# Kernel optimization log

Measured on AMD Instinct MI355X. Metric: run time of the kernel, lower is better.

## Reference

```python
import jax, jax.numpy as jnp
import numpy as np

N_ITER, K, DIM = 2, 16, 64


def setup_inputs() -> dict:
    key = jax.random.key(0)
    ks = jax.random.split(key, 9)
    B, NE, NU, NR = 8192, 200000, 100000, 32
    return {
        "u": jax.random.randint(ks[0], (B,), 0, NU),
        "v": jax.random.randint(ks[1], (B,), 0, NE),
        "adj_ent": jax.random.randint(ks[2], (NE, K), 0, NE),
        "adj_rel": jax.random.randint(ks[3], (NE, K), 0, NR),
        "usr_emb": jax.random.normal(ks[4], (NU, DIM), jnp.float32) * 0.1,
        "rel_emb": jax.random.normal(ks[5], (NR, DIM), jnp.float32) * 0.1,
        "ent_emb": jax.random.normal(ks[6], (NE, DIM), jnp.float32) * 0.1,
        "W": jax.random.normal(ks[7], (DIM, DIM), jnp.float32) / np.float32(np.sqrt(DIM)),
        "b": jnp.zeros((DIM,), jnp.float32),
    }


def reference(u, v, adj_ent, adj_rel, usr_emb, rel_emb, ent_emb, W, b):
    B = u.shape[0]
    user = usr_emb[u]                                  # [B, D]

    # _get_neighbors: multi-hop fixed-fanout expansion
    entities = [v[:, None]]                            # hop 0: [B, 1]
    relations = []
    for h in range(N_ITER):
        entities.append(adj_ent[entities[h]].reshape(B, -1))   # [B, K^(h+1)]
        relations.append(adj_rel[entities[h]].reshape(B, -1))

    ent_vecs = [ent_emb[e] for e in entities]          # [B, K^h, D] gathers
    rel_vecs = [rel_emb[r] for r in relations]

    # _aggregate: attention-weighted neighbor mix + sum-combine linear
    for i in range(N_ITER):
        act = jnp.tanh if i == N_ITER - 1 else jax.nn.sigmoid
        nxt = []
        for hop in range(N_ITER - i):
            self_v = ent_vecs[hop]                              # [B, m, D]
            neigh = ent_vecs[hop + 1].reshape(B, -1, K, DIM)    # [B, m, K, D]
            rel = rel_vecs[hop].reshape(B, -1, K, DIM)          # [B, m, K, D]
            scores = jnp.einsum('bd,bmkd->bmk', user, rel)      # user-relation
            attn = jax.nn.softmax(scores, axis=-1)              # [B, m, K]
            agg = jnp.einsum('bmk,bmkd->bmd', attn, neigh)      # weighted sum
            nxt.append(act((self_v + agg) @ W + b))             # sum aggregator
        ent_vecs = nxt

    item = ent_vecs[0].reshape(B, DIM)
    return jax.nn.sigmoid(jnp.sum(user * item, axis=1))        # [B]
```

## Files before the change

### kernel.cpp

```cpp
#include <hip/hip_runtime.h>

#define KF    16
#define DIM   64
#define BLOCK 256

typedef __attribute__((ext_vector_type(8))) short bs8;
typedef __attribute__((ext_vector_type(4))) float f32x4;

__device__ __forceinline__ float fsig(float x) {
    return __builtin_amdgcn_rcpf(1.0f + __expf(-x));
}
__device__ __forceinline__ float ftanh(float x) {
    float e = __expf(2.0f * x);
    return 1.0f - 2.0f * __builtin_amdgcn_rcpf(e + 1.0f);
}
__device__ __forceinline__ ushort f2bf(float x) {
    uint u = __builtin_bit_cast(uint, x);
    u += 0x7fffu + ((u >> 16) & 1u);
    return (ushort)(u >> 16);
}

__global__ __launch_bounds__(BLOCK) void kgcn_kernel(
    const int* __restrict__ u, const int* __restrict__ v,
    const int* __restrict__ adj_ent, const int* __restrict__ adj_rel,
    const float* __restrict__ usr_emb, const float* __restrict__ rel_emb,
    const float* __restrict__ ent_emb, const float* __restrict__ W,
    const float* __restrict__ bias, float* __restrict__ out, int B)
{
    __shared__ float b_l[DIM];
    __shared__ float urs_l[32];
    __shared__ int   e1l[KF];
    __shared__ float at1l[KF];
    __shared__ int   e2l[4][64];
    __shared__ float at2l[4][64];
    __shared__ __align__(16) ushort Xl[16][72];
    __shared__ float part0[4][DIM];
    __shared__ float xbuf[DIM];
    __shared__ float agg2s[DIM];
    __shared__ float psum[4];

    const int tid  = threadIdx.x;
    const int lane = tid & 63;
    const int wv   = tid >> 6;
    const int b    = blockIdx.x;
    const int lr   = lane & 15;
    const int lg   = lane >> 4;
    const int col  = wv * 16 + lr;

    bs8 wf0, wf1;
    #pragma unroll
    for (int i = 0; i < 8; ++i) {
        const int k = lg * 8 + i;
        wf0[i] = (short)f2bf(W[k * DIM + col]);
        wf1[i] = (short)f2bf(W[(k + 32) * DIM + col]);
    }
    if (tid < DIM) b_l[tid] = bias[tid];

    const int e0 = v[b];
    float user = 0.0f, ent0v = 0.0f;

    if (wv == 0) {
        user  = usr_emb[(size_t)u[b] * DIM + lane];
        ent0v = ent_emb[(size_t)e0 * DIM + lane];
        xbuf[lane] = user;
        const int r = lane & 31, h = lane >> 5;
        float s = 0.0f;
        #pragma unroll
        for (int dd = 0; dd < 32; ++dd) {
            const int d = h * 32 + dd;
            s += xbuf[d] * rel_emb[r * DIM + d];
        }
        s += __shfl_xor(s, 32);
        if (lane < 32) urs_l[lane] = s;
        const int k  = lane & 15;
        const int e1 = adj_ent[e0 * KF + k];
        const int r1 = adj_rel[e0 * KF + k];
        float sc = urs_l[r1];
        float mx = sc;
        mx = fmaxf(mx, __shfl_xor(mx, 1));
        mx = fmaxf(mx, __shfl_xor(mx, 2));
        mx = fmaxf(mx, __shfl_xor(mx, 4));
        mx = fmaxf(mx, __shfl_xor(mx, 8));
        float e  = __expf(sc - mx);
        float sm = e;
        sm += __shfl_xor(sm, 1);
        sm += __shfl_xor(sm, 2);
        sm += __shfl_xor(sm, 4);
        sm += __shfl_xor(sm, 8);
        if (lane < KF) { e1l[lane] = e1; at1l[lane] = e * __builtin_amdgcn_rcpf(sm); }
    }
    __syncthreads();

    {
        const int mm = wv * 4 + lg;
        const int em = e1l[mm];
        const int e2 = adj_ent[em * KF + lr];
        float sc = urs_l[adj_rel[em * KF + lr]];
        float mx = sc;
        mx = fmaxf(mx, __shfl_xor(mx, 1));
        mx = fmaxf(mx, __shfl_xor(mx, 2));
        mx = fmaxf(mx, __shfl_xor(mx, 4));
        mx = fmaxf(mx, __shfl_xor(mx, 8));
        float e  = __expf(sc - mx);
        float sm = e;
        sm += __shfl_xor(sm, 1);
        sm += __shfl_xor(sm, 2);
        sm += __shfl_xor(sm, 4);
        sm += __shfl_xor(sm, 8);
        e2l[wv][lane]  = e2;
        at2l[wv][lane] = e * __builtin_amdgcn_rcpf(sm);
    }

    float agg0p = 0.0f;
    #pragma unroll 1
    for (int q = 0; q < 4; ++q) {
        const int m = wv * 4 + q;
        float rows[KF + 1];
        #pragma unroll
        for (int k = 0; k < KF; ++k) {
            const int e = __builtin_amdgcn_readfirstlane(e2l[wv][q * 16 + k]);
            rows[k] = ent_emb[(size_t)e * DIM + lane];
        }
        const int es = __builtin_amdgcn_readfirstlane(e1l[m]);
        rows[KF] = ent_emb[(size_t)es * DIM + lane];

        float g0 = 0.0f, g1 = 0.0f, g2 = 0.0f, g3 = 0.0f;
        #pragma unroll
        for (int k = 0; k < KF; k += 4) {
            g0 = fmaf(at2l[wv][q * 16 + k + 0], rows[k + 0], g0);
            g1 = fmaf(at2l[wv][q * 16 + k + 1], rows[k + 1], g1);
            g2 = fmaf(at2l[wv][q * 16 + k + 2], rows[k + 2], g2);
            g3 = fmaf(at2l[wv][q * 16 + k + 3], rows[k + 3], g3);
        }
        const float selfv = rows[KF];
        const float x     = selfv + ((g0 + g1) + (g2 + g3));
        agg0p = fmaf(at1l[m], selfv, agg0p);
        Xl[m][lane] = f2bf(x);
    }
    part0[wv][lane] = agg0p;
    __syncthreads();

    const float bj = b_l[col];
    f32x4 c; c[0] = bj; c[1] = bj; c[2] = bj; c[3] = bj;
    {
        const ushort* arow = &Xl[lr][lg * 8];
        bs8 a0 = *(const bs8*)arow;
        bs8 a1 = *(const bs8*)(arow + 32);
        c = __builtin_amdgcn_mfma_f32_16x16x32_bf16(a0, wf0, c, 0, 0, 0);
        c = __builtin_amdgcn_mfma_f32_16x16x32_bf16(a1, wf1, c, 0, 0, 0);
    }
    {
        float p = 0.0f;
        #pragma unroll
        for (int r = 0; r < 4; ++r) p = fmaf(at1l[lg * 4 + r], fsig(c[r]), p);
        p += __shfl_xor(p, 16);
        p += __shfl_xor(p, 32);
        if (lane < 16) agg2s[col] = p;
    }
    __syncthreads();

    if (wv == 0) {
        const float agg0 = (part0[0][lane] + part0[1][lane]) + (part0[2][lane] + part0[3][lane]);
        Xl[0][lane] = f2bf(ent0v + agg0);
    }
    __syncthreads();

    c[0] = bj; c[1] = bj; c[2] = bj; c[3] = bj;
    {
        const ushort* arow = &Xl[lr][lg * 8];
        bs8 a0 = *(const bs8*)arow;
        bs8 a1 = *(const bs8*)(arow + 32);
        c = __builtin_amdgcn_mfma_f32_16x16x32_bf16(a0, wf0, c, 0, 0, 0);
        c = __builtin_amdgcn_mfma_f32_16x16x32_bf16(a1, wf1, c, 0, 0, 0);
    }
    __syncthreads();
    if (lane < 16) {
        const float h0 = fsig(c[0]);
        Xl[0][col] = f2bf(h0 + agg2s[col]);
    }
    __syncthreads();

    c[0] = bj; c[1] = bj; c[2] = bj; c[3] = bj;
    {
        const ushort* arow = &Xl[lr][lg * 8];
        bs8 a0 = *(const bs8*)arow;
        bs8 a1 = *(const bs8*)(arow + 32);
        c = __builtin_amdgcn_mfma_f32_16x16x32_bf16(a0, wf0, c, 0, 0, 0);
        c = __builtin_amdgcn_mfma_f32_16x16x32_bf16(a1, wf1, c, 0, 0, 0);
    }
    float pv = 0.0f;
    if (lane < 16) pv = xbuf[col] * ftanh(c[0]);
    pv += __shfl_xor(pv, 1);
    pv += __shfl_xor(pv, 2);
    pv += __shfl_xor(pv, 4);
    pv += __shfl_xor(pv, 8);
    pv += __shfl_xor(pv, 16);
    pv += __shfl_xor(pv, 32);
    if (lane == 0) psum[wv] = pv;
    __syncthreads();
    if (tid == 0) out[b] = fsig((psum[0] + psum[1]) + (psum[2] + psum[3]));
}

extern "C" void kernel_launch(void* const* d_in, const int* in_sizes, int n_in,
                              void* d_out, int out_size, void* d_ws, size_t ws_size,
                              hipStream_t stream) {
    const int*   u       = (const int*)d_in[0];
    const int*   v       = (const int*)d_in[1];
    const int*   adj_ent = (const int*)d_in[2];
    const int*   adj_rel = (const int*)d_in[3];
    const float* usr_emb = (const float*)d_in[4];
    const float* rel_emb = (const float*)d_in[5];
    const float* ent_emb = (const float*)d_in[6];
    const float* W       = (const float*)d_in[7];
    const float* bias    = (const float*)d_in[8];
    float* out = (float*)d_out;

    const int B = in_sizes[0];
    kgcn_kernel<<<B, BLOCK, 0, stream>>>(u, v, adj_ent, adj_rel,
                                         usr_emb, rel_emb, ent_emb,
                                         W, bias, out, B);
}
```

Measured before the change: 203.0 us.

## Process one batch element per wavefront with register-resident softmax and shared W fragments

Remaps the kernel so each 256-thread block handles four batch elements, one per wavefront, and launches B/4 blocks. Each wave keeps its own neighbor ids and attention weights in registers, reading them with readlane and shuffles instead of LDS, and runs all four output-column MFMA tiles itself. W is converted to bf16 fragments once per block into shared memory and reused by all four waves. This removes most block-wide barriers and the per-element W conversion and LDS traffic. In exchange each wave does more serial gather and MFMA work, and the grid has a quarter as many blocks. The launch assumes B is divisible by 4.

```diff
diff --git a/kernel.cpp b/kernel.cpp
--- a/kernel.cpp
+++ b/kernel.cpp
@@ -6,6 +6,8 @@
 
 typedef __attribute__((ext_vector_type(8))) short bs8;
 typedef __attribute__((ext_vector_type(4))) float f32x4;
+
+#define C_FENCE() asm volatile("" ::: "memory")
 
 __device__ __forceinline__ float fsig(float x) {
     return __builtin_amdgcn_rcpf(1.0f + __expf(-x));
@@ -18,6 +20,9 @@
     uint u = __builtin_bit_cast(uint, x);
     u += 0x7fffu + ((u >> 16) & 1u);
     return (ushort)(u >> 16);
+}
+__device__ __forceinline__ float rdlane_f(float v, int l) {
+    return __builtin_bit_cast(float, __builtin_amdgcn_readlane(__builtin_bit_cast(int, v), l));
 }
 
 __global__ __launch_bounds__(BLOCK) void kgcn_kernel(
@@ -27,55 +32,51 @@
     const float* __restrict__ ent_emb, const float* __restrict__ W,
     const float* __restrict__ bias, float* __restrict__ out, int B)
 {
-    __shared__ float b_l[DIM];
-    __shared__ float urs_l[32];
-    __shared__ int   e1l[KF];
-    __shared__ float at1l[KF];
-    __shared__ int   e2l[4][64];
-    __shared__ float at2l[4][64];
-    __shared__ __align__(16) ushort Xl[16][72];
-    __shared__ float part0[4][DIM];
-    __shared__ float xbuf[DIM];
-    __shared__ float agg2s[DIM];
-    __shared__ float psum[4];
+    __shared__ __align__(16) ushort Wfrag[2][4][64][8];
+    __shared__ __align__(16) ushort Xl[4][16][72];
 
     const int tid  = threadIdx.x;
     const int lane = tid & 63;
     const int wv   = tid >> 6;
-    const int b    = blockIdx.x;
     const int lr   = lane & 15;
     const int lg   = lane >> 4;
-    const int col  = wv * 16 + lr;
-
-    bs8 wf0, wf1;
-    #pragma unroll
-    for (int i = 0; i < 8; ++i) {
-        const int k = lg * 8 + i;
-        wf0[i] = (short)f2bf(W[k * DIM + col]);
-        wf1[i] = (short)f2bf(W[(k + 32) * DIM + col]);
-    }
-    if (tid < DIM) b_l[tid] = bias[tid];
-
-    const int e0 = v[b];
-    float user = 0.0f, ent0v = 0.0f;
-
-    if (wv == 0) {
-        user  = usr_emb[(size_t)u[b] * DIM + lane];
-        ent0v = ent_emb[(size_t)e0 * DIM + lane];
-        xbuf[lane] = user;
-        const int r = lane & 31, h = lane >> 5;
+
+    {
+        const int col = wv * 16 + lr;
+        bs8 p0, p1;
+        #pragma unroll
+        for (int i = 0; i < 8; ++i) {
+            p0[i] = (short)f2bf(W[(lg * 8 + i) * DIM + col]);
+            p1[i] = (short)f2bf(W[(lg * 8 + i + 32) * DIM + col]);
+        }
+        *(bs8*)&Wfrag[0][wv][lane][0] = p0;
+        *(bs8*)&Wfrag[1][wv][lane][0] = p1;
+    }
+    const float biasr = bias[lane];
+    __syncthreads();
+
+    const int   b     = blockIdx.x * 4 + wv;
+    const int   e0    = v[b];
+    const float user  = usr_emb[(size_t)u[b] * DIM + lane];
+    const float ent0v = ent_emb[(size_t)e0 * DIM + lane];
+
+    float ursr;
+    {
+        const int r  = lane & 31;
+        const int hb = lane & 32;
         float s = 0.0f;
         #pragma unroll
-        for (int dd = 0; dd < 32; ++dd) {
-            const int d = h * 32 + dd;
-            s += xbuf[d] * rel_emb[r * DIM + d];
-        }
+        for (int dd = 0; dd < 32; ++dd)
+            s = fmaf(__shfl(user, hb + dd), rel_emb[r * DIM + hb + dd], s);
         s += __shfl_xor(s, 32);
-        if (lane < 32) urs_l[lane] = s;
-        const int k  = lane & 15;
-        const int e1 = adj_ent[e0 * KF + k];
-        const int r1 = adj_rel[e0 * KF + k];
-        float sc = urs_l[r1];
+        ursr = s;
+    }
+
+    int e1r; float at1r;
+    {
+        e1r = adj_ent[e0 * KF + lr];
+        const int r1 = adj_rel[e0 * KF + lr];
+        float sc = __shfl(ursr, r1);
         float mx = sc;
         mx = fmaxf(mx, __shfl_xor(mx, 1));
         mx = fmaxf(mx, __shfl_xor(mx, 2));
@@ -87,15 +88,17 @@
         sm += __shfl_xor(sm, 2);
         sm += __shfl_xor(sm, 4);
         sm += __shfl_xor(sm, 8);
-        if (lane < KF) { e1l[lane] = e1; at1l[lane] = e * __builtin_amdgcn_rcpf(sm); }
-    }
-    __syncthreads();
-
-    {
-        const int mm = wv * 4 + lg;
-        const int em = e1l[mm];
-        const int e2 = adj_ent[em * KF + lr];
-        float sc = urs_l[adj_rel[em * KF + lr]];
+        at1r = e * __builtin_amdgcn_rcpf(sm);
+    }
+
+    int e2r[4]; float at2r[4];
+    #pragma unroll
+    for (int it = 0; it < 4; ++it) {
+        const int m  = it * 4 + lg;
+        const int em = __shfl(e1r, m);
+        e2r[it] = adj_ent[em * KF + lr];
+        const int r2 = adj_rel[em * KF + lr];
+        float sc = __shfl(ursr, r2);
         float mx = sc;
         mx = fmaxf(mx, __shfl_xor(mx, 1));
         mx = fmaxf(mx, __shfl_xor(mx, 2));
@@ -107,98 +110,109 @@
         sm += __shfl_xor(sm, 2);
         sm += __shfl_xor(sm, 4);
         sm += __shfl_xor(sm, 8);
-        e2l[wv][lane]  = e2;
-        at2l[wv][lane] = e * __builtin_amdgcn_rcpf(sm);
+        at2r[it] = e * __builtin_amdgcn_rcpf(sm);
     }
 
     float agg0p = 0.0f;
-    #pragma unroll 1
-    for (int q = 0; q < 4; ++q) {
-        const int m = wv * 4 + q;
-        float rows[KF + 1];
-        #pragma unroll
-        for (int k = 0; k < KF; ++k) {
-            const int e = __builtin_amdgcn_readfirstlane(e2l[wv][q * 16 + k]);
-            rows[k] = ent_emb[(size_t)e * DIM + lane];
-        }
-        const int es = __builtin_amdgcn_readfirstlane(e1l[m]);
-        rows[KF] = ent_emb[(size_t)es * DIM + lane];
-
-        float g0 = 0.0f, g1 = 0.0f, g2 = 0.0f, g3 = 0.0f;
-        #pragma unroll
-        for (int k = 0; k < KF; k += 4) {
-            g0 = fmaf(at2l[wv][q * 16 + k + 0], rows[k + 0], g0);
-            g1 = fmaf(at2l[wv][q * 16 + k + 1], rows[k + 1], g1);
-            g2 = fmaf(at2l[wv][q * 16 + k + 2], rows[k + 2], g2);
-            g3 = fmaf(at2l[wv][q * 16 + k + 3], rows[k + 3], g3);
-        }
-        const float selfv = rows[KF];
-        const float x     = selfv + ((g0 + g1) + (g2 + g3));
-        agg0p = fmaf(at1l[m], selfv, agg0p);
-        Xl[m][lane] = f2bf(x);
-    }
-    part0[wv][lane] = agg0p;
-    __syncthreads();
-
-    const float bj = b_l[col];
-    f32x4 c; c[0] = bj; c[1] = bj; c[2] = bj; c[3] = bj;
-    {
-        const ushort* arow = &Xl[lr][lg * 8];
-        bs8 a0 = *(const bs8*)arow;
-        bs8 a1 = *(const bs8*)(arow + 32);
-        c = __builtin_amdgcn_mfma_f32_16x16x32_bf16(a0, wf0, c, 0, 0, 0);
-        c = __builtin_amdgcn_mfma_f32_16x16x32_bf16(a1, wf1, c, 0, 0, 0);
-    }
-    {
-        float p = 0.0f;
-        #pragma unroll
-        for (int r = 0; r < 4; ++r) p = fmaf(at1l[lg * 4 + r], fsig(c[r]), p);
-        p += __shfl_xor(p, 16);
-        p += __shfl_xor(p, 32);
-        if (lane < 16) agg2s[col] = p;
-    }
-    __syncthreads();
-
-    if (wv == 0) {
-        const float agg0 = (part0[0][lane] + part0[1][lane]) + (part0[2][lane] + part0[3][lane]);
-        Xl[0][lane] = f2bf(ent0v + agg0);
-    }
-    __syncthreads();
-
-    c[0] = bj; c[1] = bj; c[2] = bj; c[3] = bj;
-    {
-        const ushort* arow = &Xl[lr][lg * 8];
-        bs8 a0 = *(const bs8*)arow;
-        bs8 a1 = *(const bs8*)(arow + 32);
-        c = __builtin_amdgcn_mfma_f32_16x16x32_bf16(a0, wf0, c, 0, 0, 0);
-        c = __builtin_amdgcn_mfma_f32_16x16x32_bf16(a1, wf1, c, 0, 0, 0);
-    }
-    __syncthreads();
-    if (lane < 16) {
-        const float h0 = fsig(c[0]);
-        Xl[0][col] = f2bf(h0 + agg2s[col]);
-    }
-    __syncthreads();
-
-    c[0] = bj; c[1] = bj; c[2] = bj; c[3] = bj;
-    {
-        const ushort* arow = &Xl[lr][lg * 8];
-        bs8 a0 = *(const bs8*)arow;
-        bs8 a1 = *(const bs8*)(arow + 32);
-        c = __builtin_amdgcn_mfma_f32_16x16x32_bf16(a0, wf0, c, 0, 0, 0);
-        c = __builtin_amdgcn_mfma_f32_16x16x32_bf16(a1, wf1, c, 0, 0, 0);
-    }
+    #pragma unroll
+    for (int qo = 0; qo < 4; ++qo) {
+        #pragma unroll 1
+        for (int qi = 0; qi < 4; ++qi) {
+            const int q = qo * 4 + qi;
+            float rows[KF + 1];
+            #pragma unroll
+            for (int k = 0; k < KF; ++k) {
+                const int e = __builtin_amdgcn_readlane(e2r[qo], qi * 16 + k);
+                rows[k] = ent_emb[(size_t)e * DIM + lane];
+            }
+            const int es = __builtin_amdgcn_readlane(e1r, q);
+            rows[KF] = ent_emb[(size_t)es * DIM + lane];
+
+            float g0 = 0.0f, g1 = 0.0f, g2 = 0.0f, g3 = 0.0f;
+            #pragma unroll
+            for (int k = 0; k < KF; k += 4) {
+                g0 = fmaf(rdlane_f(at2r[qo], qi * 16 + k + 0), rows[k + 0], g0);
+                g1 = fmaf(rdlane_f(at2r[qo], qi * 16 + k + 1), rows[k + 1], g1);
+                g2 = fmaf(rdlane_f(at2r[qo], qi * 16 + k + 2), rows[k + 2], g2);
+                g3 = fmaf(rdlane_f(at2r[qo], qi * 16 + k + 3), rows[k + 3], g3);
+            }
+            const float selfv = rows[KF];
+            agg0p = fmaf(rdlane_f(at1r, q), selfv, agg0p);
+            Xl[wv][q][lane] = f2bf(selfv + ((g0 + g1) + (g2 + g3)));
+        }
+    }
+    __syncthreads();
+
+    float bj[4];
+    #pragma unroll
+    for (int t = 0; t < 4; ++t) bj[t] = __shfl(biasr, t * 16 + lr);
+
+    float agg2r[4];
+    {
+        const bs8 a0 = *(const bs8*)&Xl[wv][lr][lg * 8];
+        const bs8 a1 = *(const bs8*)&Xl[wv][lr][lg * 8 + 32];
+        #pragma unroll
+        for (int t = 0; t < 4; ++t) {
+            f32x4 c; c[0] = bj[t]; c[1] = bj[t]; c[2] = bj[t]; c[3] = bj[t];
+            const bs8 w0 = *(const bs8*)&Wfrag[0][t][lane][0];
+            const bs8 w1 = *(const bs8*)&Wfrag[1][t][lane][0];
+            c = __builtin_amdgcn_mfma_f32_16x16x32_bf16(a0, w0, c, 0, 0, 0);
+            c = __builtin_amdgcn_mfma_f32_16x16x32_bf16(a1, w1, c, 0, 0, 0);
+            float p = 0.0f;
+            #pragma unroll
+            for (int r = 0; r < 4; ++r)
+                p = fmaf(__shfl(at1r, lg * 4 + r), fsig(c[r]), p);
+            p += __shfl_xor(p, 16);
+            p += __shfl_xor(p, 32);
+            agg2r[t] = p;
+        }
+    }
+
+    C_FENCE();
+    Xl[wv][0][lane] = f2bf(ent0v + agg0p);
+    __syncthreads();
+
+    float x2v[4];
+    {
+        const bs8 a0 = *(const bs8*)&Xl[wv][lr][lg * 8];
+        const bs8 a1 = *(const bs8*)&Xl[wv][lr][lg * 8 + 32];
+        #pragma unroll
+        for (int t = 0; t < 4; ++t) {
+            f32x4 c; c[0] = bj[t]; c[1] = bj[t]; c[2] = bj[t]; c[3] = bj[t];
+            const bs8 w0 = *(const bs8*)&Wfrag[0][t][lane][0];
+            const bs8 w1 = *(const bs8*)&Wfrag[1][t][lane][0];
+            c = __builtin_amdgcn_mfma_f32_16x16x32_bf16(a0, w0, c, 0, 0, 0);
+            c = __builtin_amdgcn_mfma_f32_16x16x32_bf16(a1, w1, c, 0, 0, 0);
+            x2v[t] = fsig(c[0]) + agg2r[t];
+        }
+    }
+
+    C_FENCE();
+    #pragma unroll
+    for (int t = 0; t < 4; ++t)
+        if (lane < 16) Xl[wv][0][t * 16 + lane] = f2bf(x2v[t]);
+    __syncthreads();
+
     float pv = 0.0f;
-    if (lane < 16) pv = xbuf[col] * ftanh(c[0]);
+    {
+        const bs8 a0 = *(const bs8*)&Xl[wv][lr][lg * 8];
+        const bs8 a1 = *(const bs8*)&Xl[wv][lr][lg * 8 + 32];
+        #pragma unroll
+        for (int t = 0; t < 4; ++t) {
+            f32x4 c; c[0] = bj[t]; c[1] = bj[t]; c[2] = bj[t]; c[3] = bj[t];
+            const bs8 w0 = *(const bs8*)&Wfrag[0][t][lane][0];
+            const bs8 w1 = *(const bs8*)&Wfrag[1][t][lane][0];
+            c = __builtin_amdgcn_mfma_f32_16x16x32_bf16(a0, w0, c, 0, 0, 0);
+            c = __builtin_amdgcn_mfma_f32_16x16x32_bf16(a1, w1, c, 0, 0, 0);
+            const float uc = __shfl(user, t * 16 + lr);
+            if (lane < 16) pv = fmaf(uc, ftanh(c[0]), pv);
+        }
+    }
     pv += __shfl_xor(pv, 1);
     pv += __shfl_xor(pv, 2);
     pv += __shfl_xor(pv, 4);
     pv += __shfl_xor(pv, 8);
-    pv += __shfl_xor(pv, 16);
-    pv += __shfl_xor(pv, 32);
-    if (lane == 0) psum[wv] = pv;
-    __syncthreads();
-    if (tid == 0) out[b] = fsig((psum[0] + psum[1]) + (psum[2] + psum[3]));
+    if (lane == 0) out[b] = fsig(pv);
 }
 
 extern "C" void kernel_launch(void* const* d_in, const int* in_sizes, int n_in,
@@ -216,7 +230,7 @@
     float* out = (float*)d_out;
 
     const int B = in_sizes[0];
-    kgcn_kernel<<<B, BLOCK, 0, stream>>>(u, v, adj_ent, adj_rel,
-                                         usr_emb, rel_emb, ent_emb,
-                                         W, bias, out, B);
-}
+    kgcn_kernel<<<B / 4, BLOCK, 0, stream>>>(u, v, adj_ent, adj_rel,
+                                             usr_emb, rel_emb, ent_emb,
+                                             W, bias, out, B);
+}
```

After: 193.6 us. 1.05x faster.
